# Performance work log

Measured on AMD Instinct MI355X. Metric: run time of the kernel, lower is better.

## Reference

```python
import jax, jax.numpy as jnp
import numpy as np

B, S, D_IN, D_OUT, N_EXPERTS = 8, 4096, 512, 512, 8


def setup_inputs() -> dict:
    key = jax.random.key(0)
    k1, k2, k3, k4 = jax.random.split(key, 4)
    x = jax.random.normal(k1, (B, S, D_IN), dtype=jnp.float32)
    partitions = jax.random.randint(k2, (B, S), 0, N_EXPERTS, dtype=jnp.int32)
    # per-branch nn.Linear weights: [n, out_features, in_features], kaiming-ish scale
    W = jax.random.normal(k3, (N_EXPERTS, D_OUT, D_IN), dtype=jnp.float32) * 0.03
    b = jax.random.normal(k4, (N_EXPERTS, D_OUT), dtype=jnp.float32) * 0.01
    return {"x": x, "partitions": partitions, "W": W, "b": b}


def reference(x, partitions, W, b):
    # Hard token partition -> per-branch linear -> scatter combine.
    # Equivalent math to dynamic_partition + branch Linear + dynamic_stitch:
    # out[t] = x[t] @ W[p[t]].T + b[p[t]]
    in_shape = x.shape
    xf = x.reshape(-1, in_shape[-1])          # [T, d_in]
    p = partitions.reshape(-1)                # [T]
    # Compute all-expert outputs, then select per-token expert (vectorized
    # replacement for the variable-size per-partition GEMM loop).
    y = jnp.einsum('td,eod->teo', xf, W) + b[None, :, :]   # [T, n, d_out]
    out = jnp.take_along_axis(y, p[:, None, None], axis=1)[:, 0, :]  # [T, d_out]
    return out.reshape(in_shape[:-1] + (W.shape[1],))
```

## Files before the change

### kernel.cpp

```cpp
#include <hip/hip_runtime.h>
#include <hip/hip_bf16.h>

#define N_EXPERTS 8
#define T_TOKENS 32768
#define D 512
#define TILE 128
#define BK 64
#define NT 4
#define LT_MAX 256
#define GEMM_GRID (N_EXPERTS * LT_MAX * NT)
#define GRID_WG 1056
#define SCATTER_BLOCKS (T_TOKENS / 256)
#define CONVW_BLOCKS ((N_EXPERTS * D * D) / (8 * 256))

typedef __bf16 bf16x8 __attribute__((ext_vector_type(8)));
typedef float  f32x4  __attribute__((ext_vector_type(4)));
typedef unsigned short u16x8 __attribute__((ext_vector_type(8)));

__device__ __forceinline__ unsigned short f2bf(float f) {
    unsigned int u = __float_as_uint(f);
    u += 0x7FFFu + ((u >> 16) & 1u);
    return (unsigned short)(u >> 16);
}

__device__ __forceinline__ u16x8 cvt8(float4 a, float4 b) {
    u16x8 o;
    o[0] = f2bf(a.x); o[1] = f2bf(a.y); o[2] = f2bf(a.z); o[3] = f2bf(a.w);
    o[4] = f2bf(b.x); o[5] = f2bf(b.y); o[6] = f2bf(b.z); o[7] = f2bf(b.w);
    return o;
}

__device__ __forceinline__ void gl2lds16(const void* g, void* l) {
    __builtin_amdgcn_global_load_lds(
        (const __attribute__((address_space(1))) void*)g,
        (__attribute__((address_space(3))) void*)l, 16, 0, 0);
}

__global__ __launch_bounds__(256) void prep_kernel(
        const int* __restrict__ p, int* __restrict__ fill, int* __restrict__ sorted,
        const float* __restrict__ W, unsigned short* __restrict__ Wb) {
    int bid = blockIdx.x;
    int tid = threadIdx.x;
    if (bid < SCATTER_BLOCKS) {
        __shared__ int lcount[N_EXPERTS];
        __shared__ int lbase[N_EXPERTS];
        if (tid < N_EXPERTS) lcount[tid] = 0;
        __syncthreads();
        int t = bid * 256 + tid;
        int e = p[t];
        int lrank = atomicAdd(&lcount[e], 1);
        __syncthreads();
        if (tid < N_EXPERTS)
            lbase[tid] = (lcount[tid] > 0) ? atomicAdd(&fill[tid], lcount[tid]) : 0;
        __syncthreads();
        sorted[e * T_TOKENS + (lbase[e] + 1 + lrank)] = t;
    } else {
        size_t i = ((size_t)(bid - SCATTER_BLOCKS) * 256 + tid) * 8;
        float4 a = *(const float4*)(W + i);
        float4 b = *(const float4*)(W + i + 4);
        *(u16x8*)&Wb[i] = cvt8(a, b);
    }
}

__global__ __launch_bounds__(256, 3) void moe_gemm_rs(
        const float* __restrict__ x, const unsigned short* __restrict__ Wb,
        const float* __restrict__ bias, const int* __restrict__ fill,
        const int* __restrict__ sorted, float* __restrict__ out) {
    __shared__ int s_idx[TILE];
    __shared__ unsigned short sB[2][TILE * BK];

    int bid = blockIdx.x;
    int w6 = bid >> 3;
    int m = (bid & 7) + (w6 >> 2) * 8;
    int bn = w6 & 3;

    int e = 0, lt = 0, tacc = 0, found = 0, cnt_e = 0;
#pragma unroll
    for (int i = 0; i < N_EXPERTS; i++) {
        int c = fill[i] + 1;
        int tiles = (c + TILE - 1) >> 7;
        if (!found && m < tacc + tiles) { e = i; lt = m - tacc; cnt_e = c; found = 1; }
        tacc += tiles;
    }
    if (!found) return;
    int row0 = lt * TILE;

    int tid = threadIdx.x;
    if (tid < TILE) {
        int r = row0 + tid;
        s_idx[tid] = (r < cnt_e) ? sorted[e * T_TOKENS + r] : -1;
    }
    __syncthreads();

    int wave = tid >> 6, lane = tid & 63;
    int lrow = lane & 15, lq = lane >> 4;
    int srow = lane >> 3, scol = lane & 7, swz = scol ^ srow;

    const float* ax[2];
#pragma unroll
    for (int mb = 0; mb < 2; mb++) {
        int tok = s_idx[wave * 32 + mb * 16 + lrow];
        ax[mb] = x + (size_t)(tok < 0 ? 0 : tok) * D + lq * 8;
    }
    const unsigned short* gB = Wb + (size_t)e * D * D
                             + (size_t)(bn * TILE + wave * 32 + srow) * D + swz * 8;

#define STAGE_B(K, KB) do {                                                   \
    _Pragma("unroll") for (int t = 0; t < 4; t++)                             \
        gl2lds16(gB + (size_t)(t * 8) * D + (K) * BK,                         \
                 &sB[KB][(wave * 32 + t * 8) * BK]);                          \
} while (0)

#define LOAD_A(K, SB) do {                                                    \
    _Pragma("unroll") for (int mb = 0; mb < 2; mb++)                          \
    _Pragma("unroll") for (int ks = 0; ks < 2; ks++) {                        \
        raw[SB][mb][ks][0] = *(const float4*)(ax[mb] + (K) * BK + ks * 32);   \
        raw[SB][mb][ks][1] = *(const float4*)(ax[mb] + (K) * BK + ks * 32 + 4);\
    }                                                                         \
} while (0)

    float4 raw[2][2][2][2];
    f32x4 acc[2][8];
#pragma unroll
    for (int mb = 0; mb < 2; mb++)
#pragma unroll
        for (int nj = 0; nj < 8; nj++)
            acc[mb][nj] = (f32x4){0.f, 0.f, 0.f, 0.f};

    STAGE_B(0, 0);
    __builtin_amdgcn_sched_barrier(0);
    LOAD_A(0, 0);
    __builtin_amdgcn_sched_barrier(0);

#pragma unroll
    for (int step = 0; step < 8; step++) {
        asm volatile("s_waitcnt lgkmcnt(0)" ::: "memory");
        __builtin_amdgcn_s_barrier();
        __builtin_amdgcn_sched_barrier(0);
        if (step < 7) {
            STAGE_B(step + 1, (step + 1) & 1);
            __builtin_amdgcn_sched_barrier(0);
            asm volatile("s_waitcnt vmcnt(4)" ::: "memory");
        } else {
            asm volatile("s_waitcnt vmcnt(0)" ::: "memory");
        }
        __builtin_amdgcn_sched_barrier(0);
        bf16x8 af[2][2];
#pragma unroll
        for (int mb = 0; mb < 2; mb++)
#pragma unroll
            for (int ks = 0; ks < 2; ks++) {
                u16x8 t = cvt8(raw[step & 1][mb][ks][0], raw[step & 1][mb][ks][1]);
                af[mb][ks] = *(bf16x8*)&t;
            }
        if (step < 7) {
            LOAD_A(step + 1, (step + 1) & 1);
            __builtin_amdgcn_sched_barrier(0);
        }
        __builtin_amdgcn_s_barrier();
        __builtin_amdgcn_sched_barrier(0);
        const unsigned short* sBc = sB[step & 1];
        __builtin_amdgcn_s_setprio(1);
#pragma unroll
        for (int ks = 0; ks < 2; ks++) {
            bf16x8 bfr[8];
#pragma unroll
            for (int nj = 0; nj < 8; nj++) {
                int row = 16 * nj + lrow;
                int cb = (ks * 4 + lq) ^ (lrow & 7);
                bfr[nj] = *(const bf16x8*)&sBc[row * BK + cb * 8];
            }
#pragma unroll
            for (int mb = 0; mb < 2; mb++)
#pragma unroll
                for (int nj = 0; nj < 8; nj++)
                    acc[mb][nj] = __builtin_amdgcn_mfma_f32_16x16x32_bf16(
                        af[mb][ks], bfr[nj], acc[mb][nj], 0, 0, 0);
        }
        __builtin_amdgcn_s_setprio(0);
    }
#undef STAGE_B
#undef LOAD_A

#pragma unroll
    for (int nj = 0; nj < 8; nj++) {
        float bv = bias[e * D + bn * TILE + 16 * nj + lrow];
#pragma unroll
        for (int mb = 0; mb < 2; mb++)
#pragma unroll
            for (int r = 0; r < 4; r++)
                acc[mb][nj][r] += bv;
    }

    float* ct = (float*)&sB[0][0];
#pragma unroll
    for (int p = 0; p < 2; p++) {
        asm volatile("s_waitcnt lgkmcnt(0)" ::: "memory");
        __builtin_amdgcn_s_barrier();
        if ((wave >> 1) == p) {
#pragma unroll
            for (int mb = 0; mb < 2; mb++)
#pragma unroll
                for (int nj = 0; nj < 8; nj++)
#pragma unroll
                    for (int r = 0; r < 4; r++)
                        ct[((wave & 1) * 32 + 16 * mb + lq * 4 + r) * TILE
                           + 16 * nj + lrow] = acc[mb][nj][r];
        }
        asm volatile("s_waitcnt lgkmcnt(0)" ::: "memory");
        __builtin_amdgcn_s_barrier();
#pragma unroll
        for (int k = 0; k < 8; k++) {
            int u = tid + 256 * k;
            int row = u >> 5, ch = u & 31;
            int tok = s_idx[p * 64 + row];
            f32x4 v = *(const f32x4*)&ct[row * TILE + ch * 4];
            if (tok >= 0)
                *(f32x4*)&out[(size_t)tok * D + bn * TILE + ch * 4] = v;
        }
    }
}

__global__ __launch_bounds__(256) void moe_gemm_f32(
        const float* __restrict__ x, const float* __restrict__ W,
        const float* __restrict__ bias, const int* __restrict__ fill,
        const int* __restrict__ sorted, float* __restrict__ out) {
    __shared__ int s_idx[TILE];
    __shared__ unsigned short sA[TILE][BK + 8];
    __shared__ unsigned short sB[TILE][BK + 8];

    int bid = blockIdx.x;
    int e = bid & 7;
    int cnt = fill[e] + 1;
    int j = bid >> 3;
    int lt = j >> 2, bn = j & 3;
    int row0 = lt * TILE;
    if (row0 >= cnt) return;

    int tid = threadIdx.x;
    if (tid < TILE) {
        int r = row0 + tid;
        s_idx[tid] = (r < cnt) ? sorted[e * T_TOKENS + r] : -1;
    }
    __syncthreads();

    const float* Wbp = W + (size_t)e * D * D + (size_t)(bn * TILE) * D;

    f32x4 acc[4][4];
#pragma unroll
    for (int i = 0; i < 4; i++)
#pragma unroll
        for (int j2 = 0; j2 < 4; j2++)
            acc[i][j2] = (f32x4){0.f, 0.f, 0.f, 0.f};

    int wave = tid >> 6, lane = tid & 63;
    int wm = (wave >> 1) * 64, wn = (wave & 1) * 64;
    int lrow = lane & 15, lq = lane >> 4;

    for (int kk = 0; kk < D; kk += BK) {
#pragma unroll
        for (int i = 0; i < 8; i++) {
            int flat = tid + i * 256;
            int r = flat >> 4, c = (flat & 15) << 2;
            int tok = s_idx[r];
            float4 v = make_float4(0.f, 0.f, 0.f, 0.f);
            if (tok >= 0) v = *(const float4*)(x + (size_t)tok * D + kk + c);
            ushort4 w4;
            w4.x = f2bf(v.x); w4.y = f2bf(v.y); w4.z = f2bf(v.z); w4.w = f2bf(v.w);
            *(ushort4*)&sA[r][c] = w4;
        }
#pragma unroll
        for (int i = 0; i < 8; i++) {
            int flat = tid + i * 256;
            int r = flat >> 4, c = (flat & 15) << 2;
            float4 v = *(const float4*)(Wbp + (size_t)r * D + kk + c);
            ushort4 w4;
            w4.x = f2bf(v.x); w4.y = f2bf(v.y); w4.z = f2bf(v.z); w4.w = f2bf(v.w);
            *(ushort4*)&sB[r][c] = w4;
        }
        __syncthreads();
#pragma unroll
        for (int ks = 0; ks < 2; ks++) {
            bf16x8 af[4], bfr[4];
#pragma unroll
            for (int i = 0; i < 4; i++)
                af[i] = *(const bf16x8*)&sA[wm + 16 * i + lrow][ks * 32 + lq * 8];
#pragma unroll
            for (int j2 = 0; j2 < 4; j2++)
                bfr[j2] = *(const bf16x8*)&sB[wn + 16 * j2 + lrow][ks * 32 + lq * 8];
#pragma unroll
            for (int i = 0; i < 4; i++)
#pragma unroll
                for (int j2 = 0; j2 < 4; j2++)
                    acc[i][j2] = __builtin_amdgcn_mfma_f32_16x16x32_bf16(
                        af[i], bfr[j2], acc[i][j2], 0, 0, 0);
        }
        __syncthreads();
    }

#pragma unroll
    for (int j2 = 0; j2 < 4; j2++) {
        int ng = bn * TILE + wn + 16 * j2 + lrow;
        float bv = bias[e * D + ng];
#pragma unroll
        for (int i = 0; i < 4; i++) {
#pragma unroll
            for (int r = 0; r < 4; r++) {
                int mrow = wm + 16 * i + lq * 4 + r;
                int tok = s_idx[mrow];
                if (tok >= 0)
                    out[(size_t)tok * D + ng] = acc[i][j2][r] + bv;
            }
        }
    }
}

extern "C" void kernel_launch(void* const* d_in, const int* in_sizes, int n_in,
                              void* d_out, int out_size, void* d_ws, size_t ws_size,
                              hipStream_t stream) {
    const float* x    = (const float*)d_in[0];
    const int*   part = (const int*)d_in[1];
    const float* W    = (const float*)d_in[2];
    const float* b    = (const float*)d_in[3];
    float* out = (float*)d_out;

    const size_t wb_elems     = (size_t)N_EXPERTS * D * D;
    const size_t sorted_elems = (size_t)N_EXPERTS * T_TOKENS;
    const size_t fast_bytes   = wb_elems * 2 + (sorted_elems + 8) * 4;
    const size_t slow_bytes   = (sorted_elems + 8) * 4;

    if (ws_size >= fast_bytes) {
        unsigned short* Wb = (unsigned short*)d_ws;
        int* sorted = (int*)(Wb + wb_elems);
        int* fill   = sorted + sorted_elems;

        hipMemsetAsync(fill, 0xFF, N_EXPERTS * sizeof(int), stream);
        prep_kernel<<<SCATTER_BLOCKS + CONVW_BLOCKS, 256, 0, stream>>>(
            part, fill, sorted, W, Wb);
        moe_gemm_rs<<<GRID_WG, 256, 0, stream>>>(x, Wb, b, fill, sorted, out);
    } else if (ws_size >= slow_bytes) {
        int* sorted = (int*)d_ws;
        int* fill   = sorted + sorted_elems;

        hipMemsetAsync(fill, 0xFF, N_EXPERTS * sizeof(int), stream);
        prep_kernel<<<SCATTER_BLOCKS, 256, 0, stream>>>(
            part, fill, sorted, W, (unsigned short*)nullptr);
        moe_gemm_f32<<<GEMM_GRID, 256, 0, stream>>>(x, W, b, fill, sorted, out);
    }
}
```

Before: 176.0 us.

## Pre-convert activations to bf16 in prep kernel and stream bf16 A in GEMM

```diff
diff --git a/kernel.cpp b/kernel.cpp
--- a/kernel.cpp
+++ b/kernel.cpp
@@ -6,12 +6,14 @@
 #define D 512
 #define TILE 128
 #define BK 64
-#define NT 4
-#define LT_MAX 256
-#define GEMM_GRID (N_EXPERTS * LT_MAX * NT)
-#define GRID_WG 1056
+#define NKK (D / BK)
+#define MT_MAX 264
+#define GRID_WG (MT_MAX * 4)
 #define SCATTER_BLOCKS (T_TOKENS / 256)
 #define CONVW_BLOCKS ((N_EXPERTS * D * D) / (8 * 256))
+#define CONVX_BLOCKS ((T_TOKENS * D) / (8 * 256))
+#define LT_MAX 256
+#define GEMM_GRID (N_EXPERTS * LT_MAX * 4)
 
 typedef __bf16 bf16x8 __attribute__((ext_vector_type(8)));
 typedef float  f32x4  __attribute__((ext_vector_type(4)));
@@ -38,7 +40,8 @@
 
 __global__ __launch_bounds__(256) void prep_kernel(
         const int* __restrict__ p, int* __restrict__ fill, int* __restrict__ sorted,
-        const float* __restrict__ W, unsigned short* __restrict__ Wb) {
+        const float* __restrict__ W, unsigned short* __restrict__ Wb,
+        const float* __restrict__ x, unsigned short* __restrict__ xb) {
     int bid = blockIdx.x;
     int tid = threadIdx.x;
     if (bid < SCATTER_BLOCKS) {
@@ -54,16 +57,21 @@
             lbase[tid] = (lcount[tid] > 0) ? atomicAdd(&fill[tid], lcount[tid]) : 0;
         __syncthreads();
         sorted[e * T_TOKENS + (lbase[e] + 1 + lrank)] = t;
-    } else {
+    } else if (bid < SCATTER_BLOCKS + CONVW_BLOCKS) {
         size_t i = ((size_t)(bid - SCATTER_BLOCKS) * 256 + tid) * 8;
         float4 a = *(const float4*)(W + i);
         float4 b = *(const float4*)(W + i + 4);
         *(u16x8*)&Wb[i] = cvt8(a, b);
-    }
-}
-
-__global__ __launch_bounds__(256, 3) void moe_gemm_rs(
-        const float* __restrict__ x, const unsigned short* __restrict__ Wb,
+    } else {
+        size_t i = ((size_t)(bid - SCATTER_BLOCKS - CONVW_BLOCKS) * 256 + tid) * 8;
+        float4 a = *(const float4*)(x + i);
+        float4 b = *(const float4*)(x + i + 4);
+        *(u16x8*)&xb[i] = cvt8(a, b);
+    }
+}
+
+__global__ __launch_bounds__(256, 4) void moe_gemm_bl(
+        const unsigned short* __restrict__ xb, const unsigned short* __restrict__ Wb,
         const float* __restrict__ bias, const int* __restrict__ fill,
         const int* __restrict__ sorted, float* __restrict__ out) {
     __shared__ int s_idx[TILE];
@@ -96,11 +104,11 @@
     int lrow = lane & 15, lq = lane >> 4;
     int srow = lane >> 3, scol = lane & 7, swz = scol ^ srow;
 
-    const float* ax[2];
+    const unsigned short* ax[2];
 #pragma unroll
     for (int mb = 0; mb < 2; mb++) {
         int tok = s_idx[wave * 32 + mb * 16 + lrow];
-        ax[mb] = x + (size_t)(tok < 0 ? 0 : tok) * D + lq * 8;
+        ax[mb] = xb + (size_t)(tok < 0 ? 0 : tok) * D + lq * 8;
     }
     const unsigned short* gB = Wb + (size_t)e * D * D
                              + (size_t)(bn * TILE + wave * 32 + srow) * D + swz * 8;
@@ -113,13 +121,11 @@
 
 #define LOAD_A(K, SB) do {                                                    \
     _Pragma("unroll") for (int mb = 0; mb < 2; mb++)                          \
-    _Pragma("unroll") for (int ks = 0; ks < 2; ks++) {                        \
-        raw[SB][mb][ks][0] = *(const float4*)(ax[mb] + (K) * BK + ks * 32);   \
-        raw[SB][mb][ks][1] = *(const float4*)(ax[mb] + (K) * BK + ks * 32 + 4);\
-    }                                                                         \
+    _Pragma("unroll") for (int ks = 0; ks < 2; ks++)                          \
+        ar[SB][mb][ks] = *(const u16x8*)(ax[mb] + (K) * BK + ks * 32);        \
 } while (0)
 
-    float4 raw[2][2][2][2];
+    u16x8 ar[2][2][2];
     f32x4 acc[2][8];
 #pragma unroll
     for (int mb = 0; mb < 2; mb++)
@@ -133,49 +139,37 @@
     __builtin_amdgcn_sched_barrier(0);
 
 #pragma unroll
-    for (int step = 0; step < 8; step++) {
+    for (int step = 0; step < NKK; step++) {
         asm volatile("s_waitcnt lgkmcnt(0)" ::: "memory");
         __builtin_amdgcn_s_barrier();
         __builtin_amdgcn_sched_barrier(0);
-        if (step < 7) {
+        if (step < NKK - 1) {
             STAGE_B(step + 1, (step + 1) & 1);
+            LOAD_A(step + 1, (step + 1) & 1);
             __builtin_amdgcn_sched_barrier(0);
-            asm volatile("s_waitcnt vmcnt(4)" ::: "memory");
+            asm volatile("s_waitcnt vmcnt(8)" ::: "memory");
         } else {
             asm volatile("s_waitcnt vmcnt(0)" ::: "memory");
         }
-        __builtin_amdgcn_sched_barrier(0);
-        bf16x8 af[2][2];
-#pragma unroll
-        for (int mb = 0; mb < 2; mb++)
-#pragma unroll
-            for (int ks = 0; ks < 2; ks++) {
-                u16x8 t = cvt8(raw[step & 1][mb][ks][0], raw[step & 1][mb][ks][1]);
-                af[mb][ks] = *(bf16x8*)&t;
-            }
-        if (step < 7) {
-            LOAD_A(step + 1, (step + 1) & 1);
-            __builtin_amdgcn_sched_barrier(0);
-        }
         __builtin_amdgcn_s_barrier();
         __builtin_amdgcn_sched_barrier(0);
-        const unsigned short* sBc = sB[step & 1];
+        const unsigned short* cB = sB[step & 1];
         __builtin_amdgcn_s_setprio(1);
 #pragma unroll
         for (int ks = 0; ks < 2; ks++) {
+            int cb = (ks * 4 + lq) ^ (lrow & 7);
             bf16x8 bfr[8];
 #pragma unroll
-            for (int nj = 0; nj < 8; nj++) {
-                int row = 16 * nj + lrow;
-                int cb = (ks * 4 + lq) ^ (lrow & 7);
-                bfr[nj] = *(const bf16x8*)&sBc[row * BK + cb * 8];
-            }
-#pragma unroll
-            for (int mb = 0; mb < 2; mb++)
+            for (int nj = 0; nj < 8; nj++)
+                bfr[nj] = *(const bf16x8*)&cB[(16 * nj + lrow) * BK + cb * 8];
+#pragma unroll
+            for (int mb = 0; mb < 2; mb++) {
+                bf16x8 a = *(bf16x8*)&ar[step & 1][mb][ks];
 #pragma unroll
                 for (int nj = 0; nj < 8; nj++)
                     acc[mb][nj] = __builtin_amdgcn_mfma_f32_16x16x32_bf16(
-                        af[mb][ks], bfr[nj], acc[mb][nj], 0, 0, 0);
+                        a, bfr[nj], acc[mb][nj], 0, 0, 0);
+            }
         }
         __builtin_amdgcn_s_setprio(0);
     }
@@ -324,27 +318,30 @@
     const float* b    = (const float*)d_in[3];
     float* out = (float*)d_out;
 
+    const size_t xb_elems     = (size_t)T_TOKENS * D;
     const size_t wb_elems     = (size_t)N_EXPERTS * D * D;
     const size_t sorted_elems = (size_t)N_EXPERTS * T_TOKENS;
-    const size_t fast_bytes   = wb_elems * 2 + (sorted_elems + 8) * 4;
+    const size_t fast_bytes   = (xb_elems + wb_elems) * 2 + (sorted_elems + 8) * 4;
     const size_t slow_bytes   = (sorted_elems + 8) * 4;
 
     if (ws_size >= fast_bytes) {
-        unsigned short* Wb = (unsigned short*)d_ws;
+        unsigned short* xb = (unsigned short*)d_ws;
+        unsigned short* Wb = xb + xb_elems;
         int* sorted = (int*)(Wb + wb_elems);
         int* fill   = sorted + sorted_elems;
 
         hipMemsetAsync(fill, 0xFF, N_EXPERTS * sizeof(int), stream);
-        prep_kernel<<<SCATTER_BLOCKS + CONVW_BLOCKS, 256, 0, stream>>>(
-            part, fill, sorted, W, Wb);
-        moe_gemm_rs<<<GRID_WG, 256, 0, stream>>>(x, Wb, b, fill, sorted, out);
+        prep_kernel<<<SCATTER_BLOCKS + CONVW_BLOCKS + CONVX_BLOCKS, 256, 0, stream>>>(
+            part, fill, sorted, W, Wb, x, xb);
+        moe_gemm_bl<<<GRID_WG, 256, 0, stream>>>(xb, Wb, b, fill, sorted, out);
     } else if (ws_size >= slow_bytes) {
         int* sorted = (int*)d_ws;
         int* fill   = sorted + sorted_elems;
 
         hipMemsetAsync(fill, 0xFF, N_EXPERTS * sizeof(int), stream);
         prep_kernel<<<SCATTER_BLOCKS, 256, 0, stream>>>(
-            part, fill, sorted, W, (unsigned short*)nullptr);
+            part, fill, sorted, (const float*)nullptr, (unsigned short*)nullptr,
+            x, (unsigned short*)nullptr);
         moe_gemm_f32<<<GEMM_GRID, 256, 0, stream>>>(x, W, b, fill, sorted, out);
     }
 }
```

Result: slower. 190.9 us (+8.4%).
